# Kernel optimization log

Measured on AMD Instinct MI355X. Metric: run time of the kernel, lower is better.

Reference implementation:

```python
import jax, jax.numpy as jnp
import numpy as np

N = 100_000      # num nodes
E = 100_000      # num hyperedges
NNZ = 1_600_000  # incidence entries (avg degree 16)
DIN = 128
DOUT = 128


def setup_inputs() -> dict:
    key = jax.random.key(0)
    k1, k2, k3, k4 = jax.random.split(key, 4)
    x = jax.random.normal(k1, (N, DIN), dtype=jnp.float32)
    weight = jax.random.normal(k2, (DIN, DOUT), dtype=jnp.float32) / np.sqrt(DIN).astype(np.float32)
    bias = jax.random.normal(k3, (DOUT,), dtype=jnp.float32) * 0.02
    hyperedge_index = jax.random.randint(k4, (2, NNZ), 0, N, dtype=jnp.int64)
    return {"x": x, "weight": weight, "bias": bias, "hyperedge_index": hyperedge_index}


def reference(x, weight, bias, hyperedge_index):
    # PyG HypergraphConv (use_attention=False, heads=1):
    #   out = D^{-1} H W B^{-1} H^T (x @ Theta) + bias, W = I (unit hyperedge weights)
    node_idx = hyperedge_index[0]  # [NNZ]
    edge_idx = hyperedge_index[1]  # [NNZ]

    h = x @ weight  # [N, DOUT]

    ones = jnp.ones((NNZ,), dtype=h.dtype)
    # node degree D_i = sum of hyperedge weights (=1) over incident hyperedges
    D = jax.ops.segment_sum(ones, node_idx, num_segments=N)   # [N]
    # hyperedge degree B_e = number of incident nodes
    B = jax.ops.segment_sum(ones, edge_idx, num_segments=E)   # [E]
    Dinv = jnp.where(D > 0, 1.0 / D, 0.0)
    Binv = jnp.where(B > 0, 1.0 / B, 0.0)

    # nodes -> hyperedges: m_e = B_e^{-1} * sum_{i in e} h_i
    e_feat = jax.ops.segment_sum(h[node_idx], edge_idx, num_segments=E) * Binv[:, None]  # [E, DOUT]
    # hyperedges -> nodes: out_i = D_i^{-1} * sum_{e ni i} m_e
    out = jax.ops.segment_sum(e_feat[edge_idx], node_idx, num_segments=N) * Dinv[:, None]  # [N, DOUT]
    return out + bias
```

## Files before the change

kernel.cpp:

```cpp
#include <hip/hip_runtime.h>

#define Nn 100000
#define Ne 100000
#define NNZC 1600000
#define NBLK 256
#define CHUNK 6250
#define BSH 8
#define BUCKW 256
#define NBK 391
#define GEMM_TOTAL 1563
#define GEMM_A 782
#define GEMM_B 781
#define FCAP 5888

typedef __attribute__((ext_vector_type(8))) short short8;
typedef __attribute__((ext_vector_type(4))) float floatx4;

__device__ inline unsigned short f2bf(float f) {
    union { float f; unsigned int i; } c; c.f = f;
    unsigned int i = c.i;
    return (unsigned short)((i + 0x7fffu + ((i >> 16) & 1u)) >> 16);
}
__device__ inline unsigned int f2bf2(float lo, float hi) {
    union { float f; unsigned int i; } a, b;
    a.f = lo; b.f = hi;
    const unsigned int x = (a.i + 0x7fffu + ((a.i >> 16) & 1u)) >> 16;
    const unsigned int y = (b.i + 0x7fffu + ((b.i >> 16) & 1u)) & 0xffff0000u;
    return x | y;
}

union FusedLds {
    unsigned short wlds[128 * 136];
    struct { int a[NBK]; int b[NBK]; } s;
};

__device__ inline void gemm_block(int gb, const float* __restrict__ x,
                                  const float* __restrict__ w,
                                  unsigned short* __restrict__ h,
                                  unsigned short* wlds, int tid) {
    const int wave = tid >> 6, lane = tid & 63;
    const int q = lane >> 4, r16 = lane & 15;

    for (int i = tid; i < 4096; i += 256) {
        const int k = i >> 5;
        const int n0 = (i & 31) << 2;
        const float4 wv = *(const float4*)(w + k * 128 + n0);
        wlds[(n0 + 0) * 136 + k] = f2bf(wv.x);
        wlds[(n0 + 1) * 136 + k] = f2bf(wv.y);
        wlds[(n0 + 2) * 136 + k] = f2bf(wv.z);
        wlds[(n0 + 3) * 136 + k] = f2bf(wv.w);
    }
    __syncthreads();

    const int row0 = gb * 64 + wave * 16;
    const int rrow = min(row0 + r16, Nn - 1);

    floatx4 acc[8];
#pragma unroll
    for (int jb = 0; jb < 8; ++jb) acc[jb] = (floatx4){0.f, 0.f, 0.f, 0.f};

    const float* ap = x + (size_t)rrow * 128 + q * 8;
#pragma unroll
    for (int kk = 0; kk < 4; ++kk) {
        const float4 a0 = *(const float4*)(ap + kk * 32);
        const float4 a1 = *(const float4*)(ap + kk * 32 + 4);
        union { unsigned int u[4]; short8 s; } xf;
        xf.u[0] = f2bf2(a0.x, a0.y);
        xf.u[1] = f2bf2(a0.z, a0.w);
        xf.u[2] = f2bf2(a1.x, a1.y);
        xf.u[3] = f2bf2(a1.z, a1.w);
        const unsigned short* wp = wlds + kk * 32 + q * 8;
#pragma unroll
        for (int jb = 0; jb < 8; ++jb) {
            const short8 wf = *(const short8*)(wp + (jb * 16 + r16) * 136);
            acc[jb] = __builtin_amdgcn_mfma_f32_16x16x32_bf16(wf, xf.s, acc[jb], 0, 0, 0);
        }
    }

    if (row0 + r16 < Nn) {
        unsigned short* hb = h + (size_t)(row0 + r16) * 128 + q * 4;
#pragma unroll
        for (int jb = 0; jb < 8; ++jb) {
            uint2 o;
            o.x = f2bf2(acc[jb][0], acc[jb][1]);
            o.y = f2bf2(acc[jb][2], acc[jb][3]);
            *(uint2*)(hb + jb * 16) = o;
        }
    }
}

__global__ __launch_bounds__(256) void hist_gemm_kernel(
        const int* __restrict__ nidx, const int* __restrict__ eidx,
        int* __restrict__ histN, int* __restrict__ histE,
        const float* __restrict__ x, const float* __restrict__ w,
        unsigned short* __restrict__ h) {
    __shared__ FusedLds sm;
    const int tid = threadIdx.x;
    if (blockIdx.x < NBLK) {
        for (int j = tid; j < NBK; j += 256) { sm.s.a[j] = 0; sm.s.b[j] = 0; }
        __syncthreads();
        const int base = blockIdx.x * CHUNK;
        for (int i = base + tid; i < base + CHUNK; i += 256) {
            atomicAdd(&sm.s.a[nidx[i] >> BSH], 1);
            atomicAdd(&sm.s.b[eidx[i] >> BSH], 1);
        }
        __syncthreads();
        for (int j = tid; j < NBK; j += 256) {
            histN[j * NBLK + blockIdx.x] = sm.s.a[j];
            histE[j * NBLK + blockIdx.x] = sm.s.b[j];
        }
    } else {
        gemm_block(blockIdx.x - NBLK, x, w, h, sm.wlds, tid);
    }
}

__global__ void scan1_kernel(int* __restrict__ histN, int* __restrict__ histE,
                             int* __restrict__ bsumN, int* __restrict__ bsumE) {
    const int arr = blockIdx.x / NBK;
    const int b = blockIdx.x % NBK;
    int* a = arr ? histE : histN;
    int* bs = arr ? bsumE : bsumN;
    const int t = threadIdx.x;
    int v = a[b * 256 + t];
    __shared__ int tmp[2][256];
    int pin = 0;
    tmp[0][t] = v;
    for (int off = 1; off < 256; off <<= 1) {
        __syncthreads();
        int val = tmp[pin][t];
        if (t >= off) val += tmp[pin][t - off];
        tmp[1 - pin][t] = val;
        pin ^= 1;
    }
    __syncthreads();
    int incl = tmp[pin][t];
    a[b * 256 + t] = incl - v;
    if (t == 255) bs[b] = incl;
}

__global__ void scan3_kernel(int* __restrict__ histN, int* __restrict__ histE,
                             const int* __restrict__ bsumN, const int* __restrict__ bsumE) {
    const int arr = blockIdx.x / NBK;
    const int b = blockIdx.x % NBK;
    int* a = arr ? histE : histN;
    const int* bs = arr ? bsumE : bsumN;
    const int t = threadIdx.x;
    int part = 0;
    for (int i = t; i < b; i += 256) part += bs[i];
    __shared__ int red[256];
    red[t] = part;
    __syncthreads();
    for (int off = 128; off > 0; off >>= 1) {
        if (t < off) red[t] += red[t + off];
        __syncthreads();
    }
    a[b * 256 + t] += red[0];
}

__global__ __launch_bounds__(256) void scatter_gemm_kernel(
        const int* __restrict__ nidx, const int* __restrict__ eidx,
        const int* __restrict__ histN, const int* __restrict__ histE,
        unsigned int* __restrict__ pairsN, unsigned int* __restrict__ pairsE,
        const float* __restrict__ x, const float* __restrict__ w,
        unsigned short* __restrict__ h) {
    __shared__ FusedLds sm;
    const int tid = threadIdx.x;
    if (blockIdx.x < NBLK) {
        const int blk = blockIdx.x;
        for (int j = tid; j < NBK; j += 256) {
            sm.s.a[j] = histN[j * NBLK + blk];
            sm.s.b[j] = histE[j * NBLK + blk];
        }
        __syncthreads();
        const int base = blk * CHUNK;
        for (int i = base + tid; i < base + CHUNK; i += 256) {
            const int n = nidx[i], e = eidx[i];
            const int pn = atomicAdd(&sm.s.a[n >> BSH], 1);
            const int pe = atomicAdd(&sm.s.b[e >> BSH], 1);
            pairsN[pn] = ((unsigned int)e << 8) | (unsigned int)(n & 255);
            pairsE[pe] = ((unsigned int)n << 8) | (unsigned int)(e & 255);
        }
    } else {
        gemm_block(GEMM_A + blockIdx.x - NBLK, x, w, h, sm.wlds, tid);
    }
}

__global__ void fine_kernel(const unsigned int* __restrict__ pairsN, const unsigned int* __restrict__ pairsE,
                            const int* __restrict__ histN, const int* __restrict__ histE,
                            int* __restrict__ offsN, int* __restrict__ offsE,
                            int* __restrict__ permN, int* __restrict__ permE) {
    const int arr = blockIdx.x / NBK;
    const int b = blockIdx.x % NBK;
    const unsigned int* pairs = arr ? pairsE : pairsN;
    const int* hist = arr ? histE : histN;
    int* offs = arr ? offsE : offsN;
    int* perm = arr ? permE : permN;
    const int t = threadIdx.x;
    const int S = hist[b * NBLK];
    const int E = (b + 1 < NBK) ? hist[(b + 1) * NBLK] : NNZC;
    __shared__ int cnt[BUCKW];
    __shared__ int tmp[2][BUCKW];
    __shared__ unsigned int cache[FCAP];
    cnt[t] = 0;
    __syncthreads();
    for (int i = S + t; i < E; i += BUCKW) {
        const unsigned int p = pairs[i];
        const int loc = i - S;
        if (loc < FCAP) cache[loc] = p;
        atomicAdd(&cnt[p & 255u], 1);
    }
    __syncthreads();
    int v = cnt[t];
    int pin = 0;
    tmp[0][t] = v;
    for (int off = 1; off < BUCKW; off <<= 1) {
        __syncthreads();
        int val = tmp[pin][t];
        if (t >= off) val += tmp[pin][t - off];
        tmp[1 - pin][t] = val;
        pin ^= 1;
    }
    __syncthreads();
    const int excl = tmp[pin][t] - v;
    const int id = b * BUCKW + t;
    if (id < 100000) offs[id] = S + excl;
    if (b == NBK - 1 && t == 0) offs[100000] = NNZC;
    __syncthreads();
    cnt[t] = excl;
    __syncthreads();
    for (int i = S + t; i < E; i += BUCKW) {
        const int loc = i - S;
        const unsigned int p = (loc < FCAP) ? cache[loc] : pairs[i];
        const int pos = S + atomicAdd(&cnt[p & 255u], 1);
        perm[pos] = (int)(p >> 8);
    }
}

__device__ inline void gather_rows(const char* __restrict__ src, const int* __restrict__ perm,
                                   int start, int end, int lane, float& ax, float& ay) {
    const unsigned int laneoff = (unsigned int)lane << 2;
    for (int s0 = start; s0 < end; s0 += 64) {
        const int m = min(end - s0, 64);
        const int myv = perm[s0 + (lane < m ? lane : 0)];
        int t = 0;
        for (; t + 7 < m; t += 8) {
            unsigned int a[8], u[8];
#pragma unroll
            for (int j = 0; j < 8; ++j)
                a[j] = ((unsigned int)__shfl(myv, t + j, 64) << 8) | laneoff;
#pragma unroll
            for (int j = 0; j < 8; ++j) u[j] = *(const unsigned int*)(src + a[j]);
#pragma unroll
            for (int j = 0; j < 8; ++j) {
                ax += __uint_as_float(u[j] << 16);
                ay += __uint_as_float(u[j] & 0xffff0000u);
            }
        }
        if (t < m) {
            unsigned int a[8], u[8];
            float f[8];
#pragma unroll
            for (int j = 0; j < 8; ++j) {
                const int idx = (t + j < m) ? t + j : t;
                f[j] = (t + j < m) ? 1.f : 0.f;
                a[j] = ((unsigned int)__shfl(myv, idx, 64) << 8) | laneoff;
            }
#pragma unroll
            for (int j = 0; j < 8; ++j) u[j] = *(const unsigned int*)(src + a[j]);
#pragma unroll
            for (int j = 0; j < 8; ++j) {
                ax += f[j] * __uint_as_float(u[j] << 16);
                ay += f[j] * __uint_as_float(u[j] & 0xffff0000u);
            }
        }
    }
}

__global__ void gather_n2e_kernel(const int* __restrict__ perm, const int* __restrict__ offs,
                                  const unsigned short* __restrict__ h,
                                  unsigned short* __restrict__ ef) {
    const int wave = threadIdx.x >> 6;
    const int lane = threadIdx.x & 63;
    const int e = blockIdx.x * 4 + wave;
    const int start = offs[e], end = offs[e + 1];
    float ax = 0.f, ay = 0.f;
    gather_rows((const char*)h, perm, start, end, lane, ax, ay);
    const int deg = end - start;
    const float binv = deg ? 1.f / (float)deg : 0.f;
    const unsigned int o = f2bf2(ax * binv, ay * binv);
    *(unsigned int*)((char*)ef + (((unsigned int)e << 8) | ((unsigned int)lane << 2))) = o;
}

__global__ void gather_e2n_kernel(const int* __restrict__ perm, const int* __restrict__ offs,
                                  const unsigned short* __restrict__ ef,
                                  const float* __restrict__ bias,
                                  float* __restrict__ out) {
    const int wave = threadIdx.x >> 6;
    const int lane = threadIdx.x & 63;
    const int n = blockIdx.x * 4 + wave;
    const int start = offs[n], end = offs[n + 1];
    float ax = 0.f, ay = 0.f;
    gather_rows((const char*)ef, perm, start, end, lane, ax, ay);
    const int deg = end - start;
    const float dinv = deg ? 1.f / (float)deg : 0.f;
    const float2 b = ((const float2*)bias)[lane];
    float2 o;
    o.x = ax * dinv + b.x;
    o.y = ay * dinv + b.y;
    *(float2*)((char*)out + (((unsigned int)n << 9) | ((unsigned int)lane << 3))) = o;
}

extern "C" void kernel_launch(void* const* d_in, const int* in_sizes, int n_in,
                              void* d_out, int out_size, void* d_ws, size_t ws_size,
                              hipStream_t stream) {
    const float* x = (const float*)d_in[0];
    const float* w = (const float*)d_in[1];
    const float* bias = (const float*)d_in[2];
    const int* hei = (const int*)d_in[3];
    const int* nidx = hei;
    const int* eidx = hei + NNZC;
    float* out = (float*)d_out;

    char* p = (char*)d_ws;
    unsigned short* h = (unsigned short*)p;  p += (size_t)Nn * 128 * 2;
    unsigned short* ef = (unsigned short*)p; p += (size_t)Ne * 128 * 2;
    int* histN = (int*)p;                    p += (size_t)NBK * NBLK * 4 + 256;
    int* histE = (int*)p;                    p += (size_t)NBK * NBLK * 4 + 256;
    int* bsumN = (int*)p;                    p += 1792;
    int* bsumE = (int*)p;                    p += 1792;
    int* offsN = (int*)p;                    p += 400128;
    int* offsE = (int*)p;                    p += 400128;
    int* permN = (int*)p;                    p += (size_t)NNZC * 4;
    int* permE = (int*)p;                    p += (size_t)NNZC * 4;
    unsigned int* pairsN = (unsigned int*)p; p += (size_t)NNZC * 4;
    unsigned int* pairsE = (unsigned int*)p; p += (size_t)NNZC * 4;

    hist_gemm_kernel<<<NBLK + GEMM_A, 256, 0, stream>>>(nidx, eidx, histN, histE, x, w, h);
    scan1_kernel<<<2 * NBK, 256, 0, stream>>>(histN, histE, bsumN, bsumE);
    scan3_kernel<<<2 * NBK, 256, 0, stream>>>(histN, histE, bsumN, bsumE);
    scatter_gemm_kernel<<<NBLK + GEMM_B, 256, 0, stream>>>(nidx, eidx, histN, histE,
                                                           pairsN, pairsE, x, w, h);
    fine_kernel<<<2 * NBK, BUCKW, 0, stream>>>(pairsN, pairsE, histN, histE,
                                               offsN, offsE, permN, permE);

    gather_n2e_kernel<<<Ne / 4, 256, 0, stream>>>(permE, offsE, h, ef);
    gather_e2n_kernel<<<Nn / 4, 256, 0, stream>>>(permN, offsN, ef, bias, out);
}
```

Baseline: 311.0 us.

## Process several consecutive segments per wave in gather kernels

Each wave now walks a contiguous range covering four consecutive CSR segments instead of one. Index loads and the 8-way unrolled row gathers run across segment boundaries, and partial sums are flushed whenever a boundary is crossed. This targets the underused unrolled batches and the padded tail iterations left by short, variable-length segments (about 16 entries each). In exchange it adds per-element boundary checks with a data-dependent while loop inside the unrolled body, and launches a quarter as many waves.

New measurement: 311.3 us. No clear change (+0.1%).

```diff
diff --git a/kernel.cpp b/kernel.cpp
--- a/kernel.cpp
+++ b/kernel.cpp
@@ -12,6 +12,7 @@
 #define GEMM_A 782
 #define GEMM_B 781
 #define FCAP 5888
+#define SEGW 4
 
 typedef __attribute__((ext_vector_type(8))) short short8;
 typedef __attribute__((ext_vector_type(4))) float floatx4;
@@ -236,78 +237,73 @@
     }
 }
 
-__device__ inline void gather_rows(const char* __restrict__ src, const int* __restrict__ perm,
-                                   int start, int end, int lane, float& ax, float& ay) {
+template <int MODE>
+__global__ __launch_bounds__(256) void gather_seg_kernel(
+        const int* __restrict__ perm, const int* __restrict__ offs,
+        const void* __restrict__ srcv, const float* __restrict__ bias,
+        void* __restrict__ outv) {
+    const int wave = threadIdx.x >> 6;
+    const int lane = threadIdx.x & 63;
+    const int e0 = __builtin_amdgcn_readfirstlane((blockIdx.x * 4 + wave) * SEGW);
+    const int start = offs[e0];
+    const int end = offs[e0 + SEGW];
     const unsigned int laneoff = (unsigned int)lane << 2;
-    for (int s0 = start; s0 < end; s0 += 64) {
-        const int m = min(end - s0, 64);
-        const int myv = perm[s0 + (lane < m ? lane : 0)];
-        int t = 0;
-        for (; t + 7 < m; t += 8) {
-            unsigned int a[8], u[8];
-#pragma unroll
-            for (int j = 0; j < 8; ++j)
-                a[j] = ((unsigned int)__shfl(myv, t + j, 64) << 8) | laneoff;
-#pragma unroll
-            for (int j = 0; j < 8; ++j) u[j] = *(const unsigned int*)(src + a[j]);
-#pragma unroll
-            for (int j = 0; j < 8; ++j) {
+    const char* src = (const char*)srcv;
+
+    float bx = 0.f, by = 0.f;
+    if (MODE == 1) {
+        const float2 b = ((const float2*)bias)[lane];
+        bx = b.x; by = b.y;
+    }
+
+    float ax = 0.f, ay = 0.f;
+    int e = e0;
+    int seg_start = start;
+    int nb = offs[e0 + 1];
+
+    auto flush = [&](int deg) {
+        const float sinv = deg ? 1.f / (float)deg : 0.f;
+        if (MODE == 0) {
+            *(unsigned int*)((char*)outv + (((unsigned int)e << 8) | laneoff)) =
+                f2bf2(ax * sinv, ay * sinv);
+        } else {
+            float2 o;
+            o.x = ax * sinv + bx;
+            o.y = ay * sinv + by;
+            *(float2*)((char*)outv + (((unsigned int)e << 9) | (laneoff << 1))) = o;
+        }
+        ax = 0.f; ay = 0.f;
+        ++e;
+    };
+
+    int myv = 0;
+    for (int i = start; i < end; i += 8) {
+        const int t = (i - start) & 63;
+        if (t == 0) myv = perm[min(i + lane, NNZC - 1)];
+        const int m = min(end - i, 8);
+        unsigned int a[8], u[8];
+#pragma unroll
+        for (int j = 0; j < 8; ++j)
+            a[j] = ((unsigned int)__shfl(myv, t + (j < m ? j : m - 1), 64) << 8) | laneoff;
+#pragma unroll
+        for (int j = 0; j < 8; ++j) u[j] = *(const unsigned int*)(src + a[j]);
+#pragma unroll
+        for (int j = 0; j < 8; ++j) {
+            if (j < m) {
+                while (i + j == nb) {
+                    flush(nb - seg_start);
+                    seg_start = nb;
+                    nb = offs[e + 1];
+                }
                 ax += __uint_as_float(u[j] << 16);
                 ay += __uint_as_float(u[j] & 0xffff0000u);
             }
         }
-        if (t < m) {
-            unsigned int a[8], u[8];
-            float f[8];
-#pragma unroll
-            for (int j = 0; j < 8; ++j) {
-                const int idx = (t + j < m) ? t + j : t;
-                f[j] = (t + j < m) ? 1.f : 0.f;
-                a[j] = ((unsigned int)__shfl(myv, idx, 64) << 8) | laneoff;
-            }
-#pragma unroll
-            for (int j = 0; j < 8; ++j) u[j] = *(const unsigned int*)(src + a[j]);
-#pragma unroll
-            for (int j = 0; j < 8; ++j) {
-                ax += f[j] * __uint_as_float(u[j] << 16);
-                ay += f[j] * __uint_as_float(u[j] & 0xffff0000u);
-            }
-        }
-    }
-}
-
-__global__ void gather_n2e_kernel(const int* __restrict__ perm, const int* __restrict__ offs,
-                                  const unsigned short* __restrict__ h,
-                                  unsigned short* __restrict__ ef) {
-    const int wave = threadIdx.x >> 6;
-    const int lane = threadIdx.x & 63;
-    const int e = blockIdx.x * 4 + wave;
-    const int start = offs[e], end = offs[e + 1];
-    float ax = 0.f, ay = 0.f;
-    gather_rows((const char*)h, perm, start, end, lane, ax, ay);
-    const int deg = end - start;
-    const float binv = deg ? 1.f / (float)deg : 0.f;
-    const unsigned int o = f2bf2(ax * binv, ay * binv);
-    *(unsigned int*)((char*)ef + (((unsigned int)e << 8) | ((unsigned int)lane << 2))) = o;
-}
-
-__global__ void gather_e2n_kernel(const int* __restrict__ perm, const int* __restrict__ offs,
-                                  const unsigned short* __restrict__ ef,
-                                  const float* __restrict__ bias,
-                                  float* __restrict__ out) {
-    const int wave = threadIdx.x >> 6;
-    const int lane = threadIdx.x & 63;
-    const int n = blockIdx.x * 4 + wave;
-    const int start = offs[n], end = offs[n + 1];
-    float ax = 0.f, ay = 0.f;
-    gather_rows((const char*)ef, perm, start, end, lane, ax, ay);
-    const int deg = end - start;
-    const float dinv = deg ? 1.f / (float)deg : 0.f;
-    const float2 b = ((const float2*)bias)[lane];
-    float2 o;
-    o.x = ax * dinv + b.x;
-    o.y = ay * dinv + b.y;
-    *(float2*)((char*)out + (((unsigned int)n << 9) | ((unsigned int)lane << 3))) = o;
+    }
+    while (e < e0 + SEGW) {
+        flush(end - seg_start);
+        seg_start = end;
+    }
 }
 
 extern "C" void kernel_launch(void* const* d_in, const int* in_sizes, int n_in,
@@ -343,6 +339,6 @@
     fine_kernel<<<2 * NBK, BUCKW, 0, stream>>>(pairsN, pairsE, histN, histE,
                                                offsN, offsE, permN, permE);
 
-    gather_n2e_kernel<<<Ne / 4, 256, 0, stream>>>(permE, offsE, h, ef);
-    gather_e2n_kernel<<<Nn / 4, 256, 0, stream>>>(permN, offsN, ef, bias, out);
-}
+    gather_seg_kernel<0><<<Ne / (4 * SEGW), 256, 0, stream>>>(permE, offsE, h, nullptr, ef);
+    gather_seg_kernel<1><<<Nn / (4 * SEGW), 256, 0, stream>>>(permN, offsN, ef, bias, out);
+}
```
